# Kernel tuning notes

Hardware: AMD Instinct MI355X
Metric: run time of the kernel (lower is better)

## Reference

```python
import jax, jax.numpy as jnp
import numpy as np

N_NODES = 131072
N_EDGES = 4194304
H1, H2 = 16, 1


def setup_inputs() -> dict:
    key = jax.random.key(0)
    k = jax.random.split(key, 6)
    x = jax.random.uniform(k[0], (N_NODES, 2), dtype=jnp.float32)
    edge_index = jax.random.randint(k[1], (2, N_EDGES), 0, N_NODES, dtype=jnp.int64)
    # GCNConv weights (glorot-ish scale) and zero biases
    W1 = jax.random.normal(k[2], (2, H1), dtype=jnp.float32) * 0.5
    b1 = jnp.zeros((H1,), dtype=jnp.float32)
    W2 = jax.random.normal(k[3], (H1, H2), dtype=jnp.float32) * 0.25
    b2 = jnp.zeros((H2,), dtype=jnp.float32)
    return {"x": x, "W1": W1, "b1": b1, "W2": W2, "b2": b2, "edge_index": edge_index}


def gcn_layer(x, W, b, src, dst, n):
    # PyG GCNConv: h = D^{-1/2} (A+I) D^{-1/2} (x W) + b  (self-loops already in src/dst)
    h = x @ W                                              # [N, F_out]
    deg = jax.ops.segment_sum(jnp.ones(dst.shape[0], h.dtype), dst, num_segments=n)
    dinv = jax.lax.rsqrt(deg)                              # deg >= 1 thanks to self-loops
    norm = dinv[src] * dinv[dst]                           # [E+N]
    out = jax.ops.segment_sum(h[src] * norm[:, None], dst, num_segments=n)
    return out + b


def reference(x, W1, b1, W2, b2, edge_index):
    n = x.shape[0]
    loops = jnp.arange(n, dtype=edge_index.dtype)
    src = jnp.concatenate([edge_index[0], loops])          # add self-loops once
    dst = jnp.concatenate([edge_index[1], loops])
    h = jax.nn.relu(gcn_layer(x, W1, b1, src, dst, n))
    h = gcn_layer(h, W2, b2, src, dst, n)                  # [N, 1]
    scores = jax.nn.sigmoid(h)
    return scores[edge_index[0]]                           # gather per-edge source score [E, 1]
```

## Files before the change

### kernel.cpp

```cpp
#include <hip/hip_runtime.h>
#include <cmath>

typedef unsigned int uint;

constexpr int N  = 131072;
constexpr int E  = 4194304;
constexpr int F  = 16;
constexpr int NB = 512;
constexpr int NBLK  = 512;
constexpr int SCT   = 512;
constexpr int CHUNK = 8192;
constexpr int EPT   = 16;
constexpr int CAPB  = 9216;
constexpr int LT    = 1024;
constexpr uint SENT = 0xFFFFFFFFu;

constexpr float S1 = 4194304.0f;
constexpr float S2 = 65536.0f;

__global__ void k_init(uint* gcnt) {
    gcnt[threadIdx.x] = 0;
}

__global__ void __launch_bounds__(SCT) k_scatter(
        const int* __restrict__ src, const int* __restrict__ dst,
        uint* __restrict__ gcnt, uint* __restrict__ part2) {
    __shared__ uint ps[NB];
    __shared__ uint gbase[NB];
    __shared__ uint vals[CHUNK];
    __shared__ uint wsum[8];
    int t = threadIdx.x, g = blockIdx.x;
    int lane = t & 63, w = t >> 6;
    ps[t] = 0;
    __syncthreads();
    int d[EPT], s[EPT];
    const int4* src4 = (const int4*)src;
    const int4* dst4 = (const int4*)dst;
    int base4 = g * (CHUNK / 4);
#pragma unroll
    for (int k = 0; k < EPT / 4; ++k) {
        int4 d4 = dst4[base4 + k * SCT + t];
        int4 s4 = src4[base4 + k * SCT + t];
        d[4 * k + 0] = d4.x; d[4 * k + 1] = d4.y; d[4 * k + 2] = d4.z; d[4 * k + 3] = d4.w;
        s[4 * k + 0] = s4.x; s[4 * k + 1] = s4.y; s[4 * k + 2] = s4.z; s[4 * k + 3] = s4.w;
        atomicAdd(&ps[d4.x >> 8], 1u);
        atomicAdd(&ps[d4.y >> 8], 1u);
        atomicAdd(&ps[d4.z >> 8], 1u);
        atomicAdd(&ps[d4.w >> 8], 1u);
    }
    __syncthreads();
    uint v = ps[t];
    uint sv = v;
#pragma unroll
    for (int off = 1; off < 64; off <<= 1) {
        uint n = __shfl_up(sv, off);
        if (lane >= off) sv += n;
    }
    if (lane == 63) wsum[w] = sv;
    gbase[t] = atomicAdd(&gcnt[t], v);
    __syncthreads();
    uint wo = 0;
    for (int i = 0; i < w; ++i) wo += wsum[i];
    sv += wo;
    uint ex = sv - v;
    __syncthreads();
    ps[t] = ex;
    __syncthreads();
#pragma unroll
    for (int k = 0; k < EPT; ++k) {
        int b = d[k] >> 8;
        uint slot = atomicAdd(&ps[b], 1u);
        vals[slot] = ((uint)s[k] << 8) | (uint)(d[k] & 255);
    }
    __syncthreads();
    int sub = lane >> 4, l16 = lane & 15;
#pragma unroll 2
    for (int pass = 0; pass < 16; ++pass) {
        int r = pass * 32 + w * 4 + sub;
        uint end = ps[r];
        uint beg = (r == 0) ? 0u : ps[r - 1];
        uint len = end - beg;
        uint gb = gbase[r];
        uint* o = part2 + (size_t)r * CAPB;
        for (uint j = l16; j < len; j += 16) {
            uint gi = gb + j;
            if (gi < (uint)CAPB) o[gi] = vals[beg + j];
        }
    }
}

__global__ void __launch_bounds__(LT) k_dy(
        uint* __restrict__ part2, const uint* __restrict__ gcnt,
        const float* __restrict__ x,
        uint* __restrict__ blen, float* __restrict__ dinv, float2* __restrict__ y) {
    __shared__ uint cw[16 * 256];
    int t = threadIdx.x, b = blockIdx.x, w = t >> 6;
#pragma unroll
    for (int k = 0; k < 4; ++k) cw[k * LT + t] = 0;
    __syncthreads();
    uint L  = gcnt[b];
    uint Lc = (L > (uint)CAPB) ? (uint)CAPB : L;
    uint Lp = (Lc + 3u) & ~3u;
    uint* p = part2 + (size_t)b * CAPB;
    uint L4 = Lc >> 2;
    const uint4* p4 = (const uint4*)p;
    for (uint i = t; i < L4; i += LT) {
        uint4 q = p4[i];
        atomicAdd(&cw[w * 256 + (q.x & 255u)], 1u);
        atomicAdd(&cw[w * 256 + (q.y & 255u)], 1u);
        atomicAdd(&cw[w * 256 + (q.z & 255u)], 1u);
        atomicAdd(&cw[w * 256 + (q.w & 255u)], 1u);
    }
    uint it = (L4 << 2) + (uint)t;
    if (it < Lc) atomicAdd(&cw[w * 256 + (p[it] & 255u)], 1u);
    uint i2 = Lc + (uint)t;
    if (i2 < Lp) p[i2] = SENT;
    if (t == 0) blen[b] = Lp;
    __syncthreads();
    if (t < 256) {
        uint c = 0;
#pragma unroll
        for (int k = 0; k < 16; ++k) c += cw[k * 256 + t];
        int node = (b << 8) + t;
        float di = rsqrtf(1.0f + (float)c);
        dinv[node] = di;
        float2 xv = ((const float2*)x)[node];
        y[node] = make_float2(di * xv.x, di * xv.y);
    }
}

__global__ void __launch_bounds__(LT) k_l1(
        const uint* __restrict__ part2, const uint* __restrict__ blen,
        const float2* __restrict__ y, const float* __restrict__ dinv,
        const float* __restrict__ W1, const float* __restrict__ b1,
        const float* __restrict__ W2, float* __restrict__ g2) {
    __shared__ int a0[16 * 256], a1[16 * 256];
    int t = threadIdx.x, b = blockIdx.x, w = t >> 6;
#pragma unroll
    for (int k = 0; k < 4; ++k) { a0[k * LT + t] = 0; a1[k * LT + t] = 0; }
    __syncthreads();
    uint L4 = blen[b] >> 2;
    const uint4* p4 = (const uint4*)(part2 + (size_t)b * CAPB);
    uint i = t;
    uint4 q = (i < L4) ? p4[i] : make_uint4(SENT, SENT, SENT, SENT);
    while (i < L4) {
        uint in = i + LT;
        uint4 qn = (in < L4) ? p4[in] : make_uint4(SENT, SENT, SENT, SENT);
        bool v0 = q.x != SENT, v1 = q.y != SENT, v2 = q.z != SENT, v3 = q.w != SENT;
        float2 y0, y1, y2, y3;
        if (v0) y0 = y[q.x >> 8];
        if (v1) y1 = y[q.y >> 8];
        if (v2) y2 = y[q.z >> 8];
        if (v3) y3 = y[q.w >> 8];
        if (v0) { atomicAdd(&a0[w * 256 + (q.x & 255u)], __float2int_rn(y0.x * S1));
                  atomicAdd(&a1[w * 256 + (q.x & 255u)], __float2int_rn(y0.y * S1)); }
        if (v1) { atomicAdd(&a0[w * 256 + (q.y & 255u)], __float2int_rn(y1.x * S1));
                  atomicAdd(&a1[w * 256 + (q.y & 255u)], __float2int_rn(y1.y * S1)); }
        if (v2) { atomicAdd(&a0[w * 256 + (q.z & 255u)], __float2int_rn(y2.x * S1));
                  atomicAdd(&a1[w * 256 + (q.z & 255u)], __float2int_rn(y2.y * S1)); }
        if (v3) { atomicAdd(&a0[w * 256 + (q.w & 255u)], __float2int_rn(y3.x * S1));
                  atomicAdd(&a1[w * 256 + (q.w & 255u)], __float2int_rn(y3.y * S1)); }
        q = qn; i = in;
    }
    __syncthreads();
    if (t < 256) {
        int s0 = 0, s1 = 0;
#pragma unroll
        for (int k = 0; k < 16; ++k) { s0 += a0[k * 256 + t]; s1 += a1[k * 256 + t]; }
        int node = (b << 8) + t;
        float di = dinv[node];
        float2 yn = y[node];
        float A0 = di * ((float)s0 * (1.0f / S1) + yn.x);
        float A1 = di * ((float)s1 * (1.0f / S1) + yn.y);
        float acc = 0.0f;
#pragma unroll
        for (int f = 0; f < F; ++f) {
            float v = fmaf(A0, W1[f], fmaf(A1, W1[F + f], b1[f]));
            acc = fmaf(fmaxf(v, 0.0f), W2[f], acc);
        }
        g2[node] = di * acc;
    }
}

__global__ void __launch_bounds__(LT) k_l2(
        const uint* __restrict__ part2, const uint* __restrict__ blen,
        const float* __restrict__ g2, const float* __restrict__ dinv,
        const float* __restrict__ b2, float* __restrict__ scores) {
    __shared__ int a[16 * 256];
    int t = threadIdx.x, b = blockIdx.x, w = t >> 6;
#pragma unroll
    for (int k = 0; k < 4; ++k) a[k * LT + t] = 0;
    __syncthreads();
    uint L4 = blen[b] >> 2;
    const uint4* p4 = (const uint4*)(part2 + (size_t)b * CAPB);
    uint i = t;
    uint4 q = (i < L4) ? p4[i] : make_uint4(SENT, SENT, SENT, SENT);
    while (i < L4) {
        uint in = i + LT;
        uint4 qn = (in < L4) ? p4[in] : make_uint4(SENT, SENT, SENT, SENT);
        bool v0 = q.x != SENT, v1 = q.y != SENT, v2 = q.z != SENT, v3 = q.w != SENT;
        float f0, f1, f2, f3;
        if (v0) f0 = g2[q.x >> 8];
        if (v1) f1 = g2[q.y >> 8];
        if (v2) f2 = g2[q.z >> 8];
        if (v3) f3 = g2[q.w >> 8];
        if (v0) atomicAdd(&a[w * 256 + (q.x & 255u)], __float2int_rn(f0 * S2));
        if (v1) atomicAdd(&a[w * 256 + (q.y & 255u)], __float2int_rn(f1 * S2));
        if (v2) atomicAdd(&a[w * 256 + (q.z & 255u)], __float2int_rn(f2 * S2));
        if (v3) atomicAdd(&a[w * 256 + (q.w & 255u)], __float2int_rn(f3 * S2));
        q = qn; i = in;
    }
    __syncthreads();
    if (t < 256) {
        int s = 0;
#pragma unroll
        for (int k = 0; k < 16; ++k) s += a[k * 256 + t];
        int node = (b << 8) + t;
        float acc = (float)s * (1.0f / S2);
        float v = fmaf(dinv[node], acc + g2[node], b2[0]);
        scores[node] = 1.0f / (1.0f + expf(-v));
    }
}

__global__ void k_out(const int* __restrict__ src, const float* __restrict__ scores,
                      float* __restrict__ out) {
    int i = blockIdx.x * blockDim.x + threadIdx.x;
    if (i >= E / 4) return;
    int4 s4 = ((const int4*)src)[i];
    float4 o;
    o.x = scores[s4.x];
    o.y = scores[s4.y];
    o.z = scores[s4.z];
    o.w = scores[s4.w];
    ((float4*)out)[i] = o;
}

extern "C" void kernel_launch(void* const* d_in, const int* in_sizes, int n_in,
                              void* d_out, int out_size, void* d_ws, size_t ws_size,
                              hipStream_t stream) {
    const float* x  = (const float*)d_in[0];
    const float* W1 = (const float*)d_in[1];
    const float* b1 = (const float*)d_in[2];
    const float* W2 = (const float*)d_in[3];
    const float* b2 = (const float*)d_in[4];
    const int*   ei = (const int*)d_in[5];
    const int* src = ei;
    const int* dst = ei + E;

    uint*   gcnt   = (uint*)d_ws;
    uint*   blen   = gcnt + NB;
    float*  dinv   = (float*)(blen + NB);
    float2* y      = (float2*)(dinv + N);
    float*  g2     = (float*)(y + N);
    float*  scores = g2 + N;
    uint*   part2  = (uint*)(scores + N);
    float*  out    = (float*)d_out;

    k_init   <<<1,             NB,  0, stream>>>(gcnt);
    k_scatter<<<NBLK,          SCT, 0, stream>>>(src, dst, gcnt, part2);
    k_dy     <<<NB,            LT,  0, stream>>>(part2, gcnt, x, blen, dinv, y);
    k_l1     <<<NB,            LT,  0, stream>>>(part2, blen, y, dinv, W1, b1, W2, g2);
    k_l2     <<<NB,            LT,  0, stream>>>(part2, blen, g2, dinv, b2, scores);
    k_out    <<<E / 4 / 256,   256, 0, stream>>>(src, scores, out);
}
```

Baseline: 169.2 us.

## Compute degrees with global atomics in scatter, drop bucket re-read kernel

The scatter kernel now counts per-node in-degree with global atomicAdds into a deg array, so the separate pass that re-read every bucket to histogram degrees becomes a light elementwise kernel. The init kernel is replaced by a memset that also zeroes the degree array. Sentinel padding moves to a single serial loop in block 0. The aim is to avoid a second full read of the partitioned edge list. The cost is 4M scattered global atomics during scatter, which may contend or slow that kernel.

```diff
diff --git a/kernel.cpp b/kernel.cpp
--- a/kernel.cpp
+++ b/kernel.cpp
@@ -18,13 +18,10 @@
 constexpr float S1 = 4194304.0f;
 constexpr float S2 = 65536.0f;
 
-__global__ void k_init(uint* gcnt) {
-    gcnt[threadIdx.x] = 0;
-}
-
 __global__ void __launch_bounds__(SCT) k_scatter(
         const int* __restrict__ src, const int* __restrict__ dst,
-        uint* __restrict__ gcnt, uint* __restrict__ part2) {
+        uint* __restrict__ gcnt, uint* __restrict__ deg,
+        uint* __restrict__ part2) {
     __shared__ uint ps[NB];
     __shared__ uint gbase[NB];
     __shared__ uint vals[CHUNK];
@@ -47,6 +44,10 @@
         atomicAdd(&ps[d4.y >> 8], 1u);
         atomicAdd(&ps[d4.z >> 8], 1u);
         atomicAdd(&ps[d4.w >> 8], 1u);
+        atomicAdd(&deg[(uint)d4.x], 1u);
+        atomicAdd(&deg[(uint)d4.y], 1u);
+        atomicAdd(&deg[(uint)d4.z], 1u);
+        atomicAdd(&deg[(uint)d4.w], 1u);
     }
     __syncthreads();
     uint v = ps[t];
@@ -84,49 +85,30 @@
         uint* o = part2 + (size_t)r * CAPB;
         for (uint j = l16; j < len; j += 16) {
             uint gi = gb + j;
-            if (gi < (uint)CAPB) o[gi] = vals[beg + j];
+            if (gi < (uint)CAPB) o[gi] = vals[gi - gb + beg];
         }
     }
 }
 
-__global__ void __launch_bounds__(LT) k_dy(
-        uint* __restrict__ part2, const uint* __restrict__ gcnt,
+__global__ void __launch_bounds__(512) k_dinvy(
+        const uint* __restrict__ gcnt, const uint* __restrict__ deg,
         const float* __restrict__ x,
-        uint* __restrict__ blen, float* __restrict__ dinv, float2* __restrict__ y) {
-    __shared__ uint cw[16 * 256];
-    int t = threadIdx.x, b = blockIdx.x, w = t >> 6;
-#pragma unroll
-    for (int k = 0; k < 4; ++k) cw[k * LT + t] = 0;
-    __syncthreads();
-    uint L  = gcnt[b];
-    uint Lc = (L > (uint)CAPB) ? (uint)CAPB : L;
-    uint Lp = (Lc + 3u) & ~3u;
-    uint* p = part2 + (size_t)b * CAPB;
-    uint L4 = Lc >> 2;
-    const uint4* p4 = (const uint4*)p;
-    for (uint i = t; i < L4; i += LT) {
-        uint4 q = p4[i];
-        atomicAdd(&cw[w * 256 + (q.x & 255u)], 1u);
-        atomicAdd(&cw[w * 256 + (q.y & 255u)], 1u);
-        atomicAdd(&cw[w * 256 + (q.z & 255u)], 1u);
-        atomicAdd(&cw[w * 256 + (q.w & 255u)], 1u);
-    }
-    uint it = (L4 << 2) + (uint)t;
-    if (it < Lc) atomicAdd(&cw[w * 256 + (p[it] & 255u)], 1u);
-    uint i2 = Lc + (uint)t;
-    if (i2 < Lp) p[i2] = SENT;
-    if (t == 0) blen[b] = Lp;
-    __syncthreads();
-    if (t < 256) {
-        uint c = 0;
-#pragma unroll
-        for (int k = 0; k < 16; ++k) c += cw[k * 256 + t];
-        int node = (b << 8) + t;
-        float di = rsqrtf(1.0f + (float)c);
-        dinv[node] = di;
-        float2 xv = ((const float2*)x)[node];
-        y[node] = make_float2(di * xv.x, di * xv.y);
-    }
+        uint* __restrict__ part2, uint* __restrict__ blen,
+        float* __restrict__ dinv, float2* __restrict__ y) {
+    int t = threadIdx.x, g = blockIdx.x;
+    if (g == 0) {
+        uint L  = gcnt[t];
+        uint Lc = (L > (uint)CAPB) ? (uint)CAPB : L;
+        uint Lp = (Lc + 3u) & ~3u;
+        uint* p = part2 + (size_t)t * CAPB;
+        for (uint i = Lc; i < Lp; ++i) p[i] = SENT;
+        blen[t] = Lp;
+    }
+    int node = g * 512 + t;
+    float di = rsqrtf(1.0f + (float)deg[node]);
+    dinv[node] = di;
+    float2 xv = ((const float2*)x)[node];
+    y[node] = make_float2(di * xv.x, di * xv.y);
 }
 
 __global__ void __launch_bounds__(LT) k_l1(
@@ -248,7 +230,8 @@
     const int* dst = ei + E;
 
     uint*   gcnt   = (uint*)d_ws;
-    uint*   blen   = gcnt + NB;
+    uint*   deg    = gcnt + NB;
+    uint*   blen   = deg + N;
     float*  dinv   = (float*)(blen + NB);
     float2* y      = (float2*)(dinv + N);
     float*  g2     = (float*)(y + N);
@@ -256,10 +239,10 @@
     uint*   part2  = (uint*)(scores + N);
     float*  out    = (float*)d_out;
 
-    k_init   <<<1,             NB,  0, stream>>>(gcnt);
-    k_scatter<<<NBLK,          SCT, 0, stream>>>(src, dst, gcnt, part2);
-    k_dy     <<<NB,            LT,  0, stream>>>(part2, gcnt, x, blen, dinv, y);
-    k_l1     <<<NB,            LT,  0, stream>>>(part2, blen, y, dinv, W1, b1, W2, g2);
-    k_l2     <<<NB,            LT,  0, stream>>>(part2, blen, g2, dinv, b2, scores);
-    k_out    <<<E / 4 / 256,   256, 0, stream>>>(src, scores, out);
-}
+    hipMemsetAsync(gcnt, 0, (size_t)(NB + N) * sizeof(uint), stream);
+    k_scatter<<<NBLK,        SCT, 0, stream>>>(src, dst, gcnt, deg, part2);
+    k_dinvy  <<<N / 512,     512, 0, stream>>>(gcnt, deg, x, part2, blen, dinv, y);
+    k_l1     <<<NB,          LT,  0, stream>>>(part2, blen, y, dinv, W1, b1, W2, g2);
+    k_l2     <<<NB,          LT,  0, stream>>>(part2, blen, g2, dinv, b2, scores);
+    k_out    <<<E / 4 / 256, 256, 0, stream>>>(src, scores, out);
+}
```

Result: slower. 321.1 us (+89.8%).
